# Kernel optimization log

Hardware: AMD Instinct MI355X
Metric: run time of the kernel (lower is better)

## Reference

```python
import jax, jax.numpy as jnp
import numpy as np

N_LEFT = 16384   # rows in left table
N_RIGHT = 16384  # rows in right table
D = 256          # columns per table


def setup_inputs() -> dict:
    key = jax.random.key(0)
    k1, k2, k3, k4 = jax.random.split(key, 4)
    left = jax.random.normal(k1, (N_LEFT, D), dtype=jnp.float32)
    right = jax.random.normal(k2, (N_RIGHT, D), dtype=jnp.float32)
    # Join keys: unique integer-valued keys (permutations of arange) so that
    # each right row matches exactly one left row -> output shape is static
    # [N_RIGHT, 2*D], matching what the torch nested-loop join would produce.
    lperm = jax.random.permutation(k3, N_LEFT).astype(jnp.float32)
    rperm = jax.random.permutation(k4, N_RIGHT).astype(jnp.float32)
    left = left.at[:, 0].set(lperm)
    right = right.at[:, 0].set(rperm)
    return {"left": left, "right": right, "left_on": 0, "right_on": 0}


def reference(left, right, left_on, right_on):
    # Vectorized equi-join. The torch module loops: for each right (outer) row,
    # scan all left rows and emit cat([left_row, right_row]) on key equality.
    # With unique keys each right row yields exactly one match, so the result
    # is, in right-row order, the matched left row concatenated with the right row.
    lkeys = left[:, left_on]                      # [N]
    rkeys = right[:, right_on]                    # [M]
    match = rkeys[:, None] == lkeys[None, :]      # [M, N] equality grid (the O(N*M) work)
    idx = jnp.argmax(match, axis=1)               # [M] index of matching left row
    joined_left = jnp.take(left, idx, axis=0)     # [M, D] gather matched left rows
    return jnp.concatenate([joined_left, right], axis=1)  # [M, 2*D]
```

## Files before the change

### kernel.cpp

```cpp
#include <hip/hip_runtime.h>


#define DCOLS 256
#define OCOLS 512

__global__ void build_table_kernel(const float* __restrict__ left,
                                   const int* __restrict__ left_on_p,
                                   int* __restrict__ table,
                                   int n_left) {
    int j = blockIdx.x * blockDim.x + threadIdx.x;
    if (j >= n_left) return;
    int key = (int)left[(size_t)j * DCOLS + left_on_p[0]];
    if (key >= 0 && key < n_left) table[key] = j;
}

__global__ void join_kernel(const float* __restrict__ left,
                            const float* __restrict__ right,
                            const int* __restrict__ right_on_p,
                            const int* __restrict__ table,
                            float* __restrict__ out,
                            int n_right) {
    int gtid = blockIdx.x * blockDim.x + threadIdx.x;
    int row  = gtid >> 6;
    int lane = threadIdx.x & 63;
    if (row >= n_right) return;

    int key = (int)right[(size_t)row * DCOLS + right_on_p[0]];
    int j   = table[key];

    const float4* lsrc = (const float4*)(left  + (size_t)j   * DCOLS);
    const float4* rsrc = (const float4*)(right + (size_t)row * DCOLS);
    float4*       o    = (float4*)(out + (size_t)row * OCOLS);

    o[lane]      = lsrc[lane];
    o[lane + 64] = rsrc[lane];
}

extern "C" void kernel_launch(void* const* d_in, const int* in_sizes, int n_in,
                              void* d_out, int out_size, void* d_ws, size_t ws_size,
                              hipStream_t stream) {
    const float* left     = (const float*)d_in[0];
    const float* right    = (const float*)d_in[1];
    const int*   left_on  = (const int*)d_in[2];
    const int*   right_on = (const int*)d_in[3];
    float*       out      = (float*)d_out;

    int n_left  = in_sizes[0] / DCOLS;
    int n_right = in_sizes[1] / DCOLS;

    int* table = (int*)d_ws;

    {
        int block = 256;
        int grid  = (n_left + block - 1) / block;
        build_table_kernel<<<grid, block, 0, stream>>>(left, left_on, table, n_left);
    }
    {
        int block = 256;
        int rows_per_block = block / 64;
        int grid = (n_right + rows_per_block - 1) / rows_per_block;
        join_kernel<<<grid, block, 0, stream>>>(right  == nullptr ? nullptr : left,
                                                right, right_on, table, out, n_right);
    }
}
```

Measured before the change: 90.43 us.

## Switch join to scatter from left rows via right-key table with nontemporal I/O

Builds the hash table over right keys instead of left keys. The join kernel then streams each left row contiguously, reads its key through a wave shuffle, and scatters it to the matching output row, while right rows are copied straight through. Nontemporal loads and stores are used to avoid cache pollution, and the table-build block size drops to 64. This removes the dependent table lookup that sat in front of the random left-row gather, in exchange for scattered writes, and it assumes keys are unique.

```diff
diff --git a/kernel.cpp b/kernel.cpp
--- a/kernel.cpp
+++ b/kernel.cpp
@@ -4,36 +4,47 @@
 #define DCOLS 256
 #define OCOLS 512
 
-__global__ void build_table_kernel(const float* __restrict__ left,
-                                   const int* __restrict__ left_on_p,
-                                   int* __restrict__ table,
-                                   int n_left) {
-    int j = blockIdx.x * blockDim.x + threadIdx.x;
-    if (j >= n_left) return;
-    int key = (int)left[(size_t)j * DCOLS + left_on_p[0]];
-    if (key >= 0 && key < n_left) table[key] = j;
+typedef float f4 __attribute__((ext_vector_type(4)));
+
+__global__ void build_rtable_kernel(const float* __restrict__ right,
+                                    const int* __restrict__ right_on_p,
+                                    int* __restrict__ rtable,
+                                    int n_right, int tsize) {
+    int i = blockIdx.x * blockDim.x + threadIdx.x;
+    if (i >= n_right) return;
+    int k = (int)right[(size_t)i * DCOLS + right_on_p[0]];
+    if (k >= 0 && k < tsize) rtable[k] = i;
 }
 
-__global__ void join_kernel(const float* __restrict__ left,
-                            const float* __restrict__ right,
-                            const int* __restrict__ right_on_p,
-                            const int* __restrict__ table,
-                            float* __restrict__ out,
-                            int n_right) {
+__global__ void scatter_join_kernel(const float* __restrict__ left,
+                                    const float* __restrict__ right,
+                                    const int* __restrict__ left_on_p,
+                                    const int* __restrict__ rtable,
+                                    float* __restrict__ out,
+                                    int n_left, int n_right, int tsize) {
     int gtid = blockIdx.x * blockDim.x + threadIdx.x;
     int row  = gtid >> 6;
     int lane = threadIdx.x & 63;
-    if (row >= n_right) return;
+    int lon  = left_on_p[0];
 
-    int key = (int)right[(size_t)row * DCOLS + right_on_p[0]];
-    int j   = table[key];
+    if (row < n_right) {
+        f4 rv = __builtin_nontemporal_load(
+                    (const f4*)(right + (size_t)row * DCOLS) + lane);
+        __builtin_nontemporal_store(rv,
+                    (f4*)(out + (size_t)row * OCOLS + DCOLS) + lane);
+    }
 
-    const float4* lsrc = (const float4*)(left  + (size_t)j   * DCOLS);
-    const float4* rsrc = (const float4*)(right + (size_t)row * DCOLS);
-    float4*       o    = (float4*)(out + (size_t)row * OCOLS);
-
-    o[lane]      = lsrc[lane];
-    o[lane + 64] = rsrc[lane];
+    if (row < n_left) {
+        f4 lv = __builtin_nontemporal_load(
+                    (const f4*)(left + (size_t)row * DCOLS) + lane);
+        float kf = ((const float*)&lv)[lon & 3];
+        float kb = __shfl(kf, lon >> 2, 64);
+        int   k  = (int)kb;
+        int dest = (k >= 0 && k < tsize) ? rtable[k] : -1;
+        if (dest >= 0 && dest < n_right)
+            __builtin_nontemporal_store(lv,
+                        (f4*)(out + (size_t)dest * OCOLS) + lane);
+    }
 }
 
 extern "C" void kernel_launch(void* const* d_in, const int* in_sizes, int n_in,
@@ -47,19 +58,23 @@
 
     int n_left  = in_sizes[0] / DCOLS;
     int n_right = in_sizes[1] / DCOLS;
+    int tsize   = n_left > n_right ? n_left : n_right;
 
-    int* table = (int*)d_ws;
+    int* rtable = (int*)d_ws;
 
     {
-        int block = 256;
-        int grid  = (n_left + block - 1) / block;
-        build_table_kernel<<<grid, block, 0, stream>>>(left, left_on, table, n_left);
+        int block = 64;
+        int grid  = (n_right + block - 1) / block;
+        build_rtable_kernel<<<grid, block, 0, stream>>>(right, right_on,
+                                                        rtable, n_right, tsize);
     }
     {
+        int rows = n_left > n_right ? n_left : n_right;
         int block = 256;
         int rows_per_block = block / 64;
-        int grid = (n_right + rows_per_block - 1) / rows_per_block;
-        join_kernel<<<grid, block, 0, stream>>>(right  == nullptr ? nullptr : left,
-                                                right, right_on, table, out, n_right);
+        int grid = (rows + rows_per_block - 1) / rows_per_block;
+        scatter_join_kernel<<<grid, block, 0, stream>>>(left, right, left_on,
+                                                        rtable, out,
+                                                        n_left, n_right, tsize);
     }
 }
```

New measurement: 93.38 us. +3.3%, slower.
